# Kernel optimization log

Measured on AMD Instinct MI355X. Metric: run time of the kernel, lower is better.

The kernel has to match this reference:

```python
import jax, jax.numpy as jnp
import numpy as np

N = 100000   # nodes
E = 1600000  # edges
H = 256      # hidden_dim
G = 64       # graphs in batch
OUT = 2      # out_dim


def setup_inputs() -> dict:
    key = jax.random.key(0)
    ks = jax.random.split(key, 20)
    f32 = jnp.float32

    def w(k, shape, fan_in):
        lim = 1.0 / np.sqrt(fan_in)
        return jax.random.uniform(k, shape, f32, -lim, lim)

    return {
        "content_x": jax.random.normal(ks[0], (N, 310), f32),
        "bert_x":    jax.random.normal(ks[1], (N, 768), f32),
        "profile_x": jax.random.normal(ks[2], (N, 10), f32),
        "spacy_x":   jax.random.normal(ks[3], (N, 300), f32),
        "edge_index": jax.random.randint(ks[4], (2, E), 0, N, dtype=jnp.int32),
        "batch":      jax.random.randint(ks[5], (N,), 0, G, dtype=jnp.int32),
        # feature-branch linears
        "Wc": w(ks[6], (310, H), 310), "bc": jnp.zeros((H,), f32),
        "Wb": w(ks[7], (768, H), 768), "bb": jnp.zeros((H,), f32),
        "Wp": w(ks[8], (10, H), 10),   "bp": jnp.zeros((H,), f32),
        "Ws": w(ks[9], (300, H), 300), "bs": jnp.zeros((H,), f32),
        # GCN conv weights (PyG GCNConv: x @ W, aggregate, + bias)
        "Wg1": w(ks[10], (4 * H, H), 4 * H), "bg1": jnp.zeros((H,), f32),
        "Wg2": w(ks[11], (H, H), H),         "bg2": jnp.zeros((H,), f32),
        # head linears
        "Wl1": w(ks[12], (H, H), H),   "bl1": jnp.zeros((H,), f32),
        "Wl2": w(ks[13], (H, OUT), H), "bl2": jnp.zeros((OUT,), f32),
    }


def gcn_conv(x, W, b, src, dst, n_nodes):
    """PyG GCNConv with added self-loops and symmetric normalization."""
    h = x @ W  # [N, out]
    # degree (dst side) including self-loop
    deg = jnp.ones((n_nodes,), h.dtype).at[dst].add(1.0)
    dinv = jax.lax.rsqrt(deg)
    coef = (dinv[src] * dinv[dst])[:, None]          # [E,1]
    agg = jax.ops.segment_sum(h[src] * coef, dst, num_segments=n_nodes)
    agg = agg + h * (dinv * dinv)[:, None]           # self-loop term
    return agg + b


def reference(content_x, bert_x, profile_x, spacy_x, edge_index, batch,
              Wc, bc, Wb, bb, Wp, bp, Ws, bs,
              Wg1, bg1, Wg2, bg2, Wl1, bl1, Wl2, bl2):
    relu = jax.nn.relu
    # multi-branch linear + relu, then concat
    out = jnp.concatenate([
        relu(content_x @ Wc + bc),
        relu(bert_x @ Wb + bb),
        relu(profile_x @ Wp + bp),
        relu(spacy_x @ Ws + bs),
    ], axis=1)  # [N, 4H]
    # dropout is identity at inference
    src, dst = edge_index[0], edge_index[1]
    out = relu(gcn_conv(out, Wg1, bg1, src, dst, N))
    out = relu(gcn_conv(out, Wg2, bg2, src, dst, N))
    # global mean pool over graphs
    ones = jnp.ones((N,), out.dtype)
    cnt = jax.ops.segment_sum(ones, batch, num_segments=G)
    pooled = jax.ops.segment_sum(out, batch, num_segments=G)
    pooled = pooled / jnp.maximum(cnt, 1.0)[:, None]  # [G, H]
    h = relu(pooled @ Wl1 + bl1)
    logits = h @ Wl2 + bl2
    return jax.nn.log_softmax(logits, axis=-1)
```

## Files before the change

kernel.cpp:

```cpp
#include <hip/hip_runtime.h>
#include <hip/hip_bf16.h>
#include <stdint.h>

#define NN 100000
#define NE 1600000
#define HID 256
#define NGRAPH 64
#define POOL_BLOCKS 256

typedef __attribute__((ext_vector_type(8))) short short8;
typedef __attribute__((ext_vector_type(4))) float f32x4;
typedef __attribute__((ext_vector_type(4))) unsigned int u32x4;

static __device__ inline float bf2f(unsigned short u){
  union { unsigned int i; float f; } x; x.i = ((unsigned int)u) << 16; return x.f;
}
static __device__ inline unsigned short f2bf(float f){
  union { float f; unsigned int i; } x; x.f = f;
  unsigned int r = x.i + 0x7fffu + ((x.i >> 16) & 1u);
  return (unsigned short)(r >> 16);
}
static __device__ inline void gload16(const void* g, void* l){
  __builtin_amdgcn_global_load_lds((const __attribute__((address_space(1))) void*)g,
                                   (__attribute__((address_space(3))) void*)l, 16, 0, 0);
}
static __device__ __forceinline__ void fence_bar_v8(){
  asm volatile("s_waitcnt vmcnt(8) lgkmcnt(0)" ::: "memory");
  __builtin_amdgcn_s_barrier(); __builtin_amdgcn_sched_barrier(0);
}
static __device__ __forceinline__ void fence_bar_v4(){
  asm volatile("s_waitcnt vmcnt(4) lgkmcnt(0)" ::: "memory");
  __builtin_amdgcn_s_barrier(); __builtin_amdgcn_sched_barrier(0);
}
static __device__ __forceinline__ void fence_bar_v0(){
  asm volatile("s_waitcnt vmcnt(0) lgkmcnt(0)" ::: "memory");
  __builtin_amdgcn_s_barrier(); __builtin_amdgcn_sched_barrier(0);
}

struct GArgs {
  const void* A;
  const unsigned short* WT;
  const float* bias;
  unsigned short* C;
  int lda, K, Kp, ldc;
};

__global__ __launch_bounds__(256) void gemmf_k(GArgs g0, GArgs g1, GArgs g2, GArgs g3, int M)
{
  __shared__ unsigned char smem[2][16384];
  GArgs g = g0;
  if (blockIdx.z == 1) g = g1;
  else if (blockIdx.z == 2) g = g2;
  else if (blockIdx.z == 3) g = g3;

  const int tid = threadIdx.x, lane = tid & 63, wid = tid >> 6;
  const int wm = wid >> 1, wn = wid & 1;
  const int bm = blockIdx.x * 128, bn = blockIdx.y * 128;
  const int l15 = lane & 15, lk = lane >> 4;
  const int K = g.K, Kp = g.Kp, lda = g.lda, NK = Kp >> 5;
  const float* Af = (const float*)g.A;

  size_t rbF[2]; int kcF[2], wbF[2];
#pragma unroll
  for (int it = 0; it < 2; ++it) {
    int cidx = it * 256 + tid, row = cidx >> 2, c = cidx & 3;
    int gr = bm + row; if (gr >= M) gr = M - 1;
    rbF[it] = (size_t)gr * lda; kcF[it] = c * 8;
    wbF[it] = row * 64 + ((c ^ ((row >> 1) & 3)) << 4);
  }
  size_t obB[2]; int ldsB[2];
#pragma unroll
  for (int it = 0; it < 2; ++it) {
    int inst = it * 4 + wid, cidx = inst * 64 + lane, row = cidx >> 2, c = cidx & 3;
    obB[it] = (size_t)(bn + row) * Kp + (c ^ ((row >> 1) & 3)) * 8;
    ldsB[it] = 8192 + inst * 1024;
  }

  float2 fvA[8], fvB[8];
  f32x4 acc[4][4];
#pragma unroll
  for (int i = 0; i < 4; i++)
#pragma unroll
    for (int j = 0; j < 4; j++) acc[i][j] = (f32x4){0.f, 0.f, 0.f, 0.f};

#define LOADF(S, k0_) do{ \
  if ((k0_) + 32 <= K) { \
    _Pragma("unroll") for (int it = 0; it < 2; ++it){ \
      const float* bp = Af + rbF[it] + (k0_) + kcF[it]; \
      _Pragma("unroll") for (int q = 0; q < 4; ++q) S[it*4+q] = *(const float2*)(bp + 2*q); \
    } \
  } else { \
    _Pragma("unroll") for (int it = 0; it < 2; ++it){ \
      const float* bp = Af + rbF[it]; \
      _Pragma("unroll") for (int q = 0; q < 4; ++q){ \
        int k = (k0_) + kcF[it] + 2*q; \
        S[it*4+q].x = (k < K) ? bp[k] : 0.f; \
        S[it*4+q].y = (k+1 < K) ? bp[k+1] : 0.f; \
      } } } } while(0)

#define CVTW(S, bufb) do{ \
  _Pragma("unroll") for (int it = 0; it < 2; ++it){ \
    u32x4 pk; \
    _Pragma("unroll") for (int q = 0; q < 4; ++q) \
      pk[q] = (unsigned)f2bf(S[it*4+q].x) | ((unsigned)f2bf(S[it*4+q].y) << 16); \
    *(u32x4*)(&smem[bufb][wbF[it]]) = pk; } } while(0)

#define STAGEB(bufb, k0_) do{ \
  _Pragma("unroll") for (int it = 0; it < 2; ++it) \
    gload16(g.WT + obB[it] + (k0_), &smem[bufb][ldsB[it]]); } while(0)

#define DOMFMA(bufb) do{ \
  short8 a[4], b[4]; \
  _Pragma("unroll") for (int i = 0; i < 4; ++i){ int row = wm*64 + i*16 + l15; \
    a[i] = *(const short8*)(&smem[bufb][row*64 + ((lk ^ ((row>>1)&3)) << 4)]); } \
  _Pragma("unroll") for (int j = 0; j < 4; ++j){ int row = wn*64 + j*16 + l15; \
    b[j] = *(const short8*)(&smem[bufb][8192 + row*64 + ((lk ^ ((row>>1)&3)) << 4)]); } \
  _Pragma("unroll") for (int i = 0; i < 4; ++i) \
    _Pragma("unroll") for (int j = 0; j < 4; ++j) \
      acc[i][j] = __builtin_amdgcn_mfma_f32_16x16x32_bf16(a[i], b[j], acc[i][j], 0, 0, 0); \
  } while(0)

  LOADF(fvA, 0);
  CVTW(fvA, 0);
  STAGEB(0, 0);
  LOADF(fvB, 32);
  fence_bar_v8();

  for (int t = 0; t < NK; t += 2) {
    { const bool h1 = (t + 1) < NK, h2 = (t + 2) < NK;
      if (h1) STAGEB(1, (t + 1) << 5);
      if (h2) LOADF(fvA, (t + 2) << 5);
      DOMFMA(0);
      if (h1) CVTW(fvB, 1);
      if (h2) fence_bar_v8(); else fence_bar_v0(); }
    { const bool h1 = (t + 2) < NK, h2 = (t + 3) < NK;
      if (h1) STAGEB(0, (t + 2) << 5);
      if (h2) LOADF(fvB, (t + 3) << 5);
      DOMFMA(1);
      if (h1) CVTW(fvA, 0);
      if (h2) fence_bar_v8(); else fence_bar_v0(); }
  }

#pragma unroll
  for (int j = 0; j < 4; j++) {
    int col = bn + wn * 64 + j * 16 + l15;
    float bv = g.bias[col];
#pragma unroll
    for (int i = 0; i < 4; i++) {
#pragma unroll
      for (int r = 0; r < 4; r++) {
        int row = bm + wm * 64 + i * 16 + lk * 4 + r;
        float v = fmaxf(acc[i][j][r] + bv, 0.f);
        unsigned u = f2bf(v);
        unsigned pu = (unsigned)__shfl_xor((int)u, 1);
        if (!(lane & 1) && row < M)
          *(unsigned*)(g.C + (size_t)row * g.ldc + col) = u | (pu << 16);
      }
    }
  }
#undef LOADF
#undef CVTW
#undef STAGEB
#undef DOMFMA
}

__global__ __launch_bounds__(256) void gemmb_k(GArgs g, int M)
{
  __shared__ unsigned char smem[49152];
  const int tid = threadIdx.x, lane = tid & 63, wid = tid >> 6;
  const int wm = wid >> 1, wn = wid & 1;
  const int bm = blockIdx.x * 128, bn = blockIdx.y * 128;
  const int l15 = lane & 15, lk = lane >> 4;
  const int Kp = g.Kp, lda = g.lda, NK = Kp >> 5;
  const unsigned short* Ab = (const unsigned short*)g.A;

  size_t obA[2], obB[2]; int ldsA[2], ldsB[2];
#pragma unroll
  for (int it = 0; it < 2; ++it) {
    int inst = it * 4 + wid, cidx = inst * 64 + lane, row = cidx >> 2, c = cidx & 3;
    int gr = bm + row; if (gr >= M) gr = M - 1;
    obA[it] = (size_t)gr * lda + (c ^ ((row >> 1) & 3)) * 8;
    ldsA[it] = inst * 1024;
    obB[it] = (size_t)(bn + row) * Kp + (c ^ ((row >> 1) & 3)) * 8;
    ldsB[it] = 8192 + inst * 1024;
  }

  f32x4 acc[4][4];
#pragma unroll
  for (int i = 0; i < 4; i++)
#pragma unroll
    for (int j = 0; j < 4; j++) acc[i][j] = (f32x4){0.f, 0.f, 0.f, 0.f};

#define STAGE3(ob_, k0_) do{ \
  _Pragma("unroll") for (int it = 0; it < 2; ++it) \
    gload16(Ab + obA[it] + (k0_), smem + (ob_) + ldsA[it]); \
  _Pragma("unroll") for (int it = 0; it < 2; ++it) \
    gload16(g.WT + obB[it] + (k0_), smem + (ob_) + ldsB[it]); } while(0)

  STAGE3(0, 0);
  STAGE3(16384, 32);
  fence_bar_v4();
  int o0 = 0, o1 = 16384, o2 = 32768;

  for (int t = 0; t < NK; ++t) {
    const bool h2 = (t + 2) < NK;
    if (h2) STAGE3(o2, (t + 2) << 5);
    short8 a[4], b[4];
#pragma unroll
    for (int i = 0; i < 4; ++i) { int row = wm * 64 + i * 16 + l15;
      a[i] = *(const short8*)(smem + o0 + row * 64 + ((lk ^ ((row >> 1) & 3)) << 4)); }
#pragma unroll
    for (int j = 0; j < 4; ++j) { int row = wn * 64 + j * 16 + l15;
      b[j] = *(const short8*)(smem + o0 + 8192 + row * 64 + ((lk ^ ((row >> 1) & 3)) << 4)); }
#pragma unroll
    for (int i = 0; i < 4; ++i)
#pragma unroll
      for (int j = 0; j < 4; ++j)
        acc[i][j] = __builtin_amdgcn_mfma_f32_16x16x32_bf16(a[i], b[j], acc[i][j], 0, 0, 0);
    if (h2) fence_bar_v4(); else fence_bar_v0();
    int tmp = o0; o0 = o1; o1 = o2; o2 = tmp;
  }

#pragma unroll
  for (int j = 0; j < 4; j++) {
    int col = bn + wn * 64 + j * 16 + l15;
#pragma unroll
    for (int i = 0; i < 4; i++) {
#pragma unroll
      for (int r = 0; r < 4; r++) {
        int row = bm + wm * 64 + i * 16 + lk * 4 + r;
        unsigned u = f2bf(acc[i][j][r]);
        unsigned pu = (unsigned)__shfl_xor((int)u, 1);
        if (!(lane & 1) && row < M)
          *(unsigned*)(g.C + (size_t)row * g.ldc + col) = u | (pu << 16);
      }
    }
  }
#undef STAGE3
}

__global__ void wconv_k(const float* __restrict__ W, unsigned short* __restrict__ WT,
                        int K, int Kp)
{
  int idx = blockIdx.x * 256 + threadIdx.x;
  if (idx >= 256 * Kp) return;
  int n = idx / Kp, k = idx - n * Kp;
  float v = (k < K) ? W[(size_t)k * 256 + n] : 0.f;
  WT[(size_t)n * Kp + k] = f2bf(v);
}

__global__ void zero_int_k(int* p, int n){
  int i = blockIdx.x * 256 + threadIdx.x; if (i < n) p[i] = 0;
}
__global__ void count_k(const int* __restrict__ dst, int* __restrict__ cnt, int n){
  int e = blockIdx.x * 256 + threadIdx.x; if (e < n) atomicAdd(&cnt[dst[e]], 1);
}
__global__ void deg_k(const int* __restrict__ cnt, float* __restrict__ dinv,
                      float* __restrict__ selfc, int n){
  int i = blockIdx.x * 256 + threadIdx.x;
  if (i < n) { float d = 1.0f + (float)cnt[i]; dinv[i] = rsqrtf(d); selfc[i] = 1.0f / d; }
}
__global__ void scan1_k(const int* __restrict__ cnt, int* __restrict__ bsum, int n){
  __shared__ int s[256];
  int b = blockIdx.x, t = threadIdx.x;
  int base = b * 1024 + t * 4, v = 0;
#pragma unroll
  for (int j = 0; j < 4; j++) { int i = base + j; if (i < n) v += cnt[i]; }
  s[t] = v; __syncthreads();
  for (int o = 128; o > 0; o >>= 1) { if (t < o) s[t] += s[t + o]; __syncthreads(); }
  if (t == 0) bsum[b] = s[0];
}
__global__ void scan2_k(int* bsum, int nb){
  __shared__ int s[256];
  int t = threadIdx.x;
  int v = (t < nb) ? bsum[t] : 0;
  s[t] = v; __syncthreads();
  for (int o = 1; o < 256; o <<= 1) {
    int x = (t >= o) ? s[t - o] : 0; __syncthreads();
    s[t] += x; __syncthreads();
  }
  if (t < nb) bsum[t] = s[t] - v;
}
__global__ void scan3_k(const int* __restrict__ cnt, const int* __restrict__ bsum,
                        int* __restrict__ rowstart, int* __restrict__ cursor, int n){
  __shared__ int s[256];
  int b = blockIdx.x, t = threadIdx.x;
  int base = b * 1024 + t * 4;
  int c0 = 0, c1 = 0, c2 = 0, c3 = 0;
  if (base + 0 < n) c0 = cnt[base + 0];
  if (base + 1 < n) c1 = cnt[base + 1];
  if (base + 2 < n) c2 = cnt[base + 2];
  if (base + 3 < n) c3 = cnt[base + 3];
  int ts = c0 + c1 + c2 + c3;
  s[t] = ts; __syncthreads();
  for (int o = 1; o < 256; o <<= 1) {
    int x = (t >= o) ? s[t - o] : 0; __syncthreads();
    s[t] += x; __syncthreads();
  }
  int run = bsum[b] + s[t] - ts;
  int cc[4] = {c0, c1, c2, c3};
#pragma unroll
  for (int j = 0; j < 4; j++) {
    int i = base + j;
    if (i < n) {
      rowstart[i] = run; cursor[i] = run; run += cc[j];
      if (i == n - 1) rowstart[n] = run;
    }
  }
}
__global__ void scatter_k(const int* __restrict__ src, const int* __restrict__ dst,
                          const float* __restrict__ dinv, int* __restrict__ cursor,
                          int* __restrict__ csr_src, float* __restrict__ csr_coef, int n){
  int e = blockIdx.x * 256 + threadIdx.x; if (e >= n) return;
  int d = dst[e], s = src[e];
  int p = atomicAdd(&cursor[d], 1);
  csr_src[p] = s;
  csr_coef[p] = dinv[s] * dinv[d];
}

__global__ __launch_bounds__(256) void agg_k(
    const unsigned short* __restrict__ h,
    const int* __restrict__ rowstart, const int* __restrict__ csr_src,
    const float* __restrict__ csr_coef, const float* __restrict__ selfc,
    const float* __restrict__ bias, unsigned short* __restrict__ out)
{
  int dst = blockIdx.x * 4 + (threadIdx.x >> 6);
  if (dst >= NN) return;
  int lane = threadIdx.x & 63;
  int colb = lane * 4;
  const unsigned short* hb = h + colb;
  ushort4 hv = *(const ushort4*)(hb + (size_t)dst * 256);
  float sc = selfc[dst];
  float a0 = sc * bf2f(hv.x), a1 = sc * bf2f(hv.y), a2 = sc * bf2f(hv.z), a3 = sc * bf2f(hv.w);
  int e0 = rowstart[dst], e1 = rowstart[dst + 1];
  int e = e0;
  for (; e + 8 <= e1; e += 8) {
    int ss[8]; float cc[8]; ushort4 vv[8];
#pragma unroll
    for (int q = 0; q < 8; ++q) { ss[q] = csr_src[e + q]; cc[q] = csr_coef[e + q]; }
#pragma unroll
    for (int q = 0; q < 8; ++q) vv[q] = *(const ushort4*)(hb + (size_t)ss[q] * 256);
#pragma unroll
    for (int q = 0; q < 8; ++q) {
      a0 += cc[q] * bf2f(vv[q].x); a1 += cc[q] * bf2f(vv[q].y);
      a2 += cc[q] * bf2f(vv[q].z); a3 += cc[q] * bf2f(vv[q].w);
    }
  }
  for (; e + 2 <= e1; e += 2) {
    int s0 = csr_src[e], s1 = csr_src[e + 1];
    float c0 = csr_coef[e], c1 = csr_coef[e + 1];
    ushort4 v0 = *(const ushort4*)(hb + (size_t)s0 * 256);
    ushort4 v1 = *(const ushort4*)(hb + (size_t)s1 * 256);
    a0 += c0 * bf2f(v0.x) + c1 * bf2f(v1.x); a1 += c0 * bf2f(v0.y) + c1 * bf2f(v1.y);
    a2 += c0 * bf2f(v0.z) + c1 * bf2f(v1.z); a3 += c0 * bf2f(v0.w) + c1 * bf2f(v1.w);
  }
  if (e < e1) {
    int s0 = csr_src[e]; float c0 = csr_coef[e];
    ushort4 v0 = *(const ushort4*)(hb + (size_t)s0 * 256);
    a0 += c0 * bf2f(v0.x); a1 += c0 * bf2f(v0.y); a2 += c0 * bf2f(v0.z); a3 += c0 * bf2f(v0.w);
  }
  float4 bv = *(const float4*)(bias + colb);
  a0 = fmaxf(a0 + bv.x, 0.f); a1 = fmaxf(a1 + bv.y, 0.f);
  a2 = fmaxf(a2 + bv.z, 0.f); a3 = fmaxf(a3 + bv.w, 0.f);
  ushort4 o; o.x = f2bf(a0); o.y = f2bf(a1); o.z = f2bf(a2); o.w = f2bf(a3);
  *(ushort4*)(out + (size_t)dst * 256 + colb) = o;
}

__global__ __launch_bounds__(256) void pool_k(
    const unsigned short* __restrict__ x, const int* __restrict__ batch,
    float* __restrict__ pp, float* __restrict__ cp)
{
  __shared__ float acc[NGRAPH][HID];
  __shared__ float cl[NGRAPH];
  int t = threadIdx.x, b = blockIdx.x;
  for (int i = t; i < NGRAPH * HID; i += 256) ((float*)acc)[i] = 0.f;
  if (t < NGRAPH) cl[t] = 0.f;
  __syncthreads();
  int per = (NN + POOL_BLOCKS - 1) / POOL_BLOCKS;
  int i0 = b * per, i1 = min(NN, i0 + per);
  for (int i = i0; i < i1; ++i) {
    int g = batch[i];
    acc[g][t] += bf2f(x[(size_t)i * 256 + t]);
    if (t == 0) cl[g] += 1.f;
  }
  __syncthreads();
  for (int g = 0; g < NGRAPH; ++g) pp[(size_t)b * (NGRAPH * HID) + g * HID + t] = acc[g][t];
  if (t < NGRAPH) cp[b * NGRAPH + t] = cl[t];
}

__global__ __launch_bounds__(256) void head_k(
    const float* __restrict__ pp, const float* __restrict__ cp,
    const float* __restrict__ Wl1, const float* __restrict__ bl1,
    const float* __restrict__ Wl2, const float* __restrict__ bl2,
    float* __restrict__ out)
{
  __shared__ float pooled[HID];
  __shared__ float red[2][4];
  int g = blockIdx.x, t = threadIdx.x;
  float s = 0.f;
  for (int b = 0; b < POOL_BLOCKS; ++b) s += pp[(size_t)b * (NGRAPH * HID) + g * HID + t];
  float cnt = 0.f;
  for (int b = 0; b < POOL_BLOCKS; ++b) cnt += cp[b * NGRAPH + g];
  pooled[t] = s / fmaxf(cnt, 1.f);
  __syncthreads();
  float hv = bl1[t];
  for (int k = 0; k < HID; ++k) hv += pooled[k] * Wl1[k * HID + t];
  hv = fmaxf(hv, 0.f);
  float p0 = hv * Wl2[t * 2 + 0];
  float p1 = hv * Wl2[t * 2 + 1];
  for (int o = 32; o > 0; o >>= 1) { p0 += __shfl_down(p0, o); p1 += __shfl_down(p1, o); }
  int w = t >> 6;
  if ((t & 63) == 0) { red[0][w] = p0; red[1][w] = p1; }
  __syncthreads();
  if (t == 0) {
    float l0 = bl2[0], l1 = bl2[1];
#pragma unroll
    for (int i = 0; i < 4; i++) { l0 += red[0][i]; l1 += red[1][i]; }
    float m = fmaxf(l0, l1);
    float lse = m + logf(expf(l0 - m) + expf(l1 - m));
    out[g * 2 + 0] = l0 - lse;
    out[g * 2 + 1] = l1 - lse;
  }
}

extern "C" void kernel_launch(void* const* d_in, const int* in_sizes, int n_in,
                              void* d_out, int out_size, void* d_ws, size_t ws_size,
                              hipStream_t stream)
{
  const float* content = (const float*)d_in[0];
  const float* bert    = (const float*)d_in[1];
  const float* profile = (const float*)d_in[2];
  const float* spacy   = (const float*)d_in[3];
  const int*   eidx    = (const int*)d_in[4];
  const int*   batch   = (const int*)d_in[5];
  const float* Wc = (const float*)d_in[6];  const float* bc = (const float*)d_in[7];
  const float* Wb = (const float*)d_in[8];  const float* bb = (const float*)d_in[9];
  const float* Wp = (const float*)d_in[10]; const float* bp = (const float*)d_in[11];
  const float* Ws = (const float*)d_in[12]; const float* bs = (const float*)d_in[13];
  const float* Wg1 = (const float*)d_in[14]; const float* bg1 = (const float*)d_in[15];
  const float* Wg2 = (const float*)d_in[16]; const float* bg2 = (const float*)d_in[17];
  const float* Wl1 = (const float*)d_in[18]; const float* bl1 = (const float*)d_in[19];
  const float* Wl2 = (const float*)d_in[20]; const float* bl2 = (const float*)d_in[21];
  float* out = (float*)d_out;
  const int* srcp = eidx;
  const int* dstp = eidx + NE;

  const int KPC = 320, KPB = 768, KPP = 64, KPS = 320, KPG1 = 1024, KPG2 = 256;

  char* ws = (char*)d_ws;
  size_t off = 0;
  auto alloc = [&](size_t bytes) { size_t o = off; off += (bytes + 255) & ~(size_t)255; return o; };

  unsigned short* WTc  = (unsigned short*)(ws + alloc((size_t)256 * KPC * 2));
  unsigned short* WTb  = (unsigned short*)(ws + alloc((size_t)256 * KPB * 2));
  unsigned short* WTp  = (unsigned short*)(ws + alloc((size_t)256 * KPP * 2));
  unsigned short* WTs  = (unsigned short*)(ws + alloc((size_t)256 * KPS * 2));
  unsigned short* WTg1 = (unsigned short*)(ws + alloc((size_t)256 * KPG1 * 2));
  unsigned short* WTg2 = (unsigned short*)(ws + alloc((size_t)256 * KPG2 * 2));
  float* dinv    = (float*)(ws + alloc((size_t)NN * 4));
  float* selfc   = (float*)(ws + alloc((size_t)NN * 4));
  int* rowcnt    = (int*)(ws + alloc((size_t)NN * 4));
  int* rowstart  = (int*)(ws + alloc((size_t)(NN + 1) * 4));
  int* cursor    = (int*)(ws + alloc((size_t)NN * 4));
  int* csr_src   = (int*)(ws + alloc((size_t)NE * 4));
  float* csr_coef= (float*)(ws + alloc((size_t)NE * 4));
  int* bsum      = (int*)(ws + alloc(1024));
  float* pp      = (float*)(ws + alloc((size_t)POOL_BLOCKS * NGRAPH * HID * 4));
  float* cp      = (float*)(ws + alloc((size_t)POOL_BLOCKS * NGRAPH * 4));
  unsigned short* X1 = (unsigned short*)(ws + alloc((size_t)NN * 1024 * 2));
  unsigned short* H  = (unsigned short*)(ws + alloc((size_t)NN * 256 * 2));
  unsigned short* X2 = (unsigned short*)(ws + alloc((size_t)NN * 256 * 2));
  unsigned short* X3 = (unsigned short*)(ws + alloc((size_t)NN * 256 * 2));
  (void)ws_size; (void)in_sizes; (void)n_in; (void)out_size;

  hipStream_t s = stream;
  const int NB = (NN + 1023) / 1024;
  const int MB = (NN + 127) / 128;

  wconv_k<<<(256 * KPC + 255) / 256, 256, 0, s>>>(Wc, WTc, 310, KPC);
  wconv_k<<<(256 * KPB + 255) / 256, 256, 0, s>>>(Wb, WTb, 768, KPB);
  wconv_k<<<(256 * KPP + 255) / 256, 256, 0, s>>>(Wp, WTp, 10, KPP);
  wconv_k<<<(256 * KPS + 255) / 256, 256, 0, s>>>(Ws, WTs, 300, KPS);
  wconv_k<<<(256 * KPG1 + 255) / 256, 256, 0, s>>>(Wg1, WTg1, 1024, KPG1);
  wconv_k<<<(256 * KPG2 + 255) / 256, 256, 0, s>>>(Wg2, WTg2, 256, KPG2);

  zero_int_k<<<(NN + 255) / 256, 256, 0, s>>>(rowcnt, NN);
  count_k<<<(NE + 255) / 256, 256, 0, s>>>(dstp, rowcnt, NE);
  deg_k<<<(NN + 255) / 256, 256, 0, s>>>(rowcnt, dinv, selfc, NN);
  scan1_k<<<NB, 256, 0, s>>>(rowcnt, bsum, NN);
  scan2_k<<<1, 256, 0, s>>>(bsum, NB);
  scan3_k<<<NB, 256, 0, s>>>(rowcnt, bsum, rowstart, cursor, NN);
  scatter_k<<<(NE + 255) / 256, 256, 0, s>>>(srcp, dstp, dinv, cursor, csr_src, csr_coef, NE);

  {
    GArgs gc = { content, WTc, bc, X1 + 0,   310, 310, KPC, 1024 };
    GArgs gb = { bert,    WTb, bb, X1 + 256, 768, 768, KPB, 1024 };
    GArgs gp = { profile, WTp, bp, X1 + 512, 10,  10,  KPP, 1024 };
    GArgs gs = { spacy,   WTs, bs, X1 + 768, 300, 300, KPS, 1024 };
    gemmf_k<<<dim3(MB, 2, 4), 256, 0, s>>>(gc, gb, gp, gs, NN);
  }

  {
    GArgs g1 = { X1, WTg1, nullptr, H, 1024, 1024, KPG1, 256 };
    gemmb_k<<<dim3(MB, 2, 1), 256, 0, s>>>(g1, NN);
  }
  agg_k<<<(NN + 3) / 4, 256, 0, s>>>(H, rowstart, csr_src, csr_coef, selfc, bg1, X2);

  {
    GArgs g2 = { X2, WTg2, nullptr, H, 256, 256, KPG2, 256 };
    gemmb_k<<<dim3(MB, 2, 1), 256, 0, s>>>(g2, NN);
  }
  agg_k<<<(NN + 3) / 4, 256, 0, s>>>(H, rowstart, csr_src, csr_coef, selfc, bg2, X3);

  pool_k<<<POOL_BLOCKS, 256, 0, s>>>(X3, batch, pp, cp);
  head_k<<<NGRAPH, 256, 0, s>>>(pp, cp, Wl1, bl1, Wl2, bl2, out);
}
```

Baseline: 1.544 ms.

## Load GEMM operands directly to registers instead of staging through LDS

Both GEMM kernels drop shared-memory staging and barriers. Each lane now loads its MFMA A and B fragments straight from global memory into a register double buffer, and in the fp32-input GEMM converts with the packed v_cvt_pk_bf16_f32 instruction. The grid swaps x and y so both N-tiles of a row block run next to each other for L2 reuse of A, and launch bounds raise occupancy hints. The feature GEMM is split into two launches (aligned and unaligned inputs), with vectorized 16-byte loads on the aligned pair. Risks are uncoalesced strided global loads with duplicated traffic across waves, plus register pressure.

```diff
diff --git a/kernel.cpp b/kernel.cpp
--- a/kernel.cpp
+++ b/kernel.cpp
@@ -10,7 +10,7 @@
 
 typedef __attribute__((ext_vector_type(8))) short short8;
 typedef __attribute__((ext_vector_type(4))) float f32x4;
-typedef __attribute__((ext_vector_type(4))) unsigned int u32x4;
+typedef __attribute__((ext_vector_type(2))) float f32x2;
 
 static __device__ inline float bf2f(unsigned short u){
   union { unsigned int i; float f; } x; x.i = ((unsigned int)u) << 16; return x.f;
@@ -19,22 +19,6 @@
   union { float f; unsigned int i; } x; x.f = f;
   unsigned int r = x.i + 0x7fffu + ((x.i >> 16) & 1u);
   return (unsigned short)(r >> 16);
-}
-static __device__ inline void gload16(const void* g, void* l){
-  __builtin_amdgcn_global_load_lds((const __attribute__((address_space(1))) void*)g,
-                                   (__attribute__((address_space(3))) void*)l, 16, 0, 0);
-}
-static __device__ __forceinline__ void fence_bar_v8(){
-  asm volatile("s_waitcnt vmcnt(8) lgkmcnt(0)" ::: "memory");
-  __builtin_amdgcn_s_barrier(); __builtin_amdgcn_sched_barrier(0);
-}
-static __device__ __forceinline__ void fence_bar_v4(){
-  asm volatile("s_waitcnt vmcnt(4) lgkmcnt(0)" ::: "memory");
-  __builtin_amdgcn_s_barrier(); __builtin_amdgcn_sched_barrier(0);
-}
-static __device__ __forceinline__ void fence_bar_v0(){
-  asm volatile("s_waitcnt vmcnt(0) lgkmcnt(0)" ::: "memory");
-  __builtin_amdgcn_s_barrier(); __builtin_amdgcn_sched_barrier(0);
 }
 
 struct GArgs {
@@ -45,100 +29,84 @@
   int lda, K, Kp, ldc;
 };
 
-__global__ __launch_bounds__(256) void gemmf_k(GArgs g0, GArgs g1, GArgs g2, GArgs g3, int M)
-{
-  __shared__ unsigned char smem[2][16384];
-  GArgs g = g0;
-  if (blockIdx.z == 1) g = g1;
-  else if (blockIdx.z == 2) g = g2;
-  else if (blockIdx.z == 3) g = g3;
-
+template<bool AL4>
+__global__ __launch_bounds__(256, 2) void gemmf_k(GArgs g0, GArgs g1, int M)
+{
+  GArgs g = (blockIdx.z == 0) ? g0 : g1;
   const int tid = threadIdx.x, lane = tid & 63, wid = tid >> 6;
   const int wm = wid >> 1, wn = wid & 1;
-  const int bm = blockIdx.x * 128, bn = blockIdx.y * 128;
+  const int bm = blockIdx.y * 128, bn = blockIdx.x * 128;
   const int l15 = lane & 15, lk = lane >> 4;
   const int K = g.K, Kp = g.Kp, lda = g.lda, NK = Kp >> 5;
-  const float* Af = (const float*)g.A;
-
-  size_t rbF[2]; int kcF[2], wbF[2];
-#pragma unroll
-  for (int it = 0; it < 2; ++it) {
-    int cidx = it * 256 + tid, row = cidx >> 2, c = cidx & 3;
-    int gr = bm + row; if (gr >= M) gr = M - 1;
-    rbF[it] = (size_t)gr * lda; kcF[it] = c * 8;
-    wbF[it] = row * 64 + ((c ^ ((row >> 1) & 3)) << 4);
-  }
-  size_t obB[2]; int ldsB[2];
-#pragma unroll
-  for (int it = 0; it < 2; ++it) {
-    int inst = it * 4 + wid, cidx = inst * 64 + lane, row = cidx >> 2, c = cidx & 3;
-    obB[it] = (size_t)(bn + row) * Kp + (c ^ ((row >> 1) & 3)) * 8;
-    ldsB[it] = 8192 + inst * 1024;
-  }
-
-  float2 fvA[8], fvB[8];
+  const float* __restrict__ Af = (const float*)g.A;
+  const unsigned short* __restrict__ WT = g.WT;
+  const int kb = lk * 8;
+
+  unsigned rbF[4];
+#pragma unroll
+  for (int i = 0; i < 4; ++i) {
+    int gr = bm + wm * 64 + i * 16 + l15; if (gr >= M) gr = M - 1;
+    rbF[i] = (unsigned)gr * (unsigned)lda;
+  }
+  unsigned obB[4];
+#pragma unroll
+  for (int j = 0; j < 4; ++j)
+    obB[j] = (unsigned)(bn + wn * 64 + j * 16 + l15) * (unsigned)Kp;
+
+  f32x2 a0[16], a1[16];
+  short8 b0[4], b1[4];
   f32x4 acc[4][4];
 #pragma unroll
   for (int i = 0; i < 4; i++)
 #pragma unroll
     for (int j = 0; j < 4; j++) acc[i][j] = (f32x4){0.f, 0.f, 0.f, 0.f};
 
-#define LOADF(S, k0_) do{ \
+#define LOADA(S, k0_) do{ \
   if ((k0_) + 32 <= K) { \
-    _Pragma("unroll") for (int it = 0; it < 2; ++it){ \
-      const float* bp = Af + rbF[it] + (k0_) + kcF[it]; \
-      _Pragma("unroll") for (int q = 0; q < 4; ++q) S[it*4+q] = *(const float2*)(bp + 2*q); \
+    if (AL4) { \
+      _Pragma("unroll") for (int i = 0; i < 4; ++i){ \
+        const float* p = Af + rbF[i] + (k0_) + kb; \
+        f32x4 v0 = *(const f32x4*)p, v1 = *(const f32x4*)(p + 4); \
+        S[i*4+0] = (f32x2){v0.x, v0.y}; S[i*4+1] = (f32x2){v0.z, v0.w}; \
+        S[i*4+2] = (f32x2){v1.x, v1.y}; S[i*4+3] = (f32x2){v1.z, v1.w}; } \
+    } else { \
+      _Pragma("unroll") for (int i = 0; i < 4; ++i){ \
+        const float* p = Af + rbF[i] + (k0_) + kb; \
+        _Pragma("unroll") for (int q = 0; q < 4; ++q) S[i*4+q] = *(const f32x2*)(p + 2*q); } \
     } \
   } else { \
-    _Pragma("unroll") for (int it = 0; it < 2; ++it){ \
-      const float* bp = Af + rbF[it]; \
+    _Pragma("unroll") for (int i = 0; i < 4; ++i){ \
+      const float* p = Af + rbF[i]; \
       _Pragma("unroll") for (int q = 0; q < 4; ++q){ \
-        int k = (k0_) + kcF[it] + 2*q; \
-        S[it*4+q].x = (k < K) ? bp[k] : 0.f; \
-        S[it*4+q].y = (k+1 < K) ? bp[k+1] : 0.f; \
-      } } } } while(0)
-
-#define CVTW(S, bufb) do{ \
-  _Pragma("unroll") for (int it = 0; it < 2; ++it){ \
-    u32x4 pk; \
+        int k = (k0_) + kb + 2*q; \
+        S[i*4+q].x = (k < K) ? p[k] : 0.f; \
+        S[i*4+q].y = (k + 1 < K) ? p[k+1] : 0.f; } } \
+  } } while(0)
+
+#define LOADB(S, k0_) do{ \
+  _Pragma("unroll") for (int j = 0; j < 4; ++j) \
+    S[j] = *(const short8*)(WT + obB[j] + (k0_) + kb); } while(0)
+
+#define CVTMFMA(S, B) do{ \
+  short8 af[4]; \
+  _Pragma("unroll") for (int i = 0; i < 4; ++i){ \
+    union { short8 s; unsigned u[4]; } t; \
     _Pragma("unroll") for (int q = 0; q < 4; ++q) \
-      pk[q] = (unsigned)f2bf(S[it*4+q].x) | ((unsigned)f2bf(S[it*4+q].y) << 16); \
-    *(u32x4*)(&smem[bufb][wbF[it]]) = pk; } } while(0)
-
-#define STAGEB(bufb, k0_) do{ \
-  _Pragma("unroll") for (int it = 0; it < 2; ++it) \
-    gload16(g.WT + obB[it] + (k0_), &smem[bufb][ldsB[it]]); } while(0)
-
-#define DOMFMA(bufb) do{ \
-  short8 a[4], b[4]; \
-  _Pragma("unroll") for (int i = 0; i < 4; ++i){ int row = wm*64 + i*16 + l15; \
-    a[i] = *(const short8*)(&smem[bufb][row*64 + ((lk ^ ((row>>1)&3)) << 4)]); } \
-  _Pragma("unroll") for (int j = 0; j < 4; ++j){ int row = wn*64 + j*16 + l15; \
-    b[j] = *(const short8*)(&smem[bufb][8192 + row*64 + ((lk ^ ((row>>1)&3)) << 4)]); } \
+      asm("v_cvt_pk_bf16_f32 %0, %1, %2" : "=v"(t.u[q]) : "v"(S[i*4+q].x), "v"(S[i*4+q].y)); \
+    af[i] = t.s; } \
   _Pragma("unroll") for (int i = 0; i < 4; ++i) \
     _Pragma("unroll") for (int j = 0; j < 4; ++j) \
-      acc[i][j] = __builtin_amdgcn_mfma_f32_16x16x32_bf16(a[i], b[j], acc[i][j], 0, 0, 0); \
+      acc[i][j] = __builtin_amdgcn_mfma_f32_16x16x32_bf16(af[i], B[j], acc[i][j], 0, 0, 0); \
   } while(0)
 
-  LOADF(fvA, 0);
-  CVTW(fvA, 0);
-  STAGEB(0, 0);
-  LOADF(fvB, 32);
-  fence_bar_v8();
+  LOADA(a0, 0); LOADB(b0, 0);
+  if (NK > 1) { LOADA(a1, 32); LOADB(b1, 32); }
 
   for (int t = 0; t < NK; t += 2) {
-    { const bool h1 = (t + 1) < NK, h2 = (t + 2) < NK;
-      if (h1) STAGEB(1, (t + 1) << 5);
-      if (h2) LOADF(fvA, (t + 2) << 5);
-      DOMFMA(0);
-      if (h1) CVTW(fvB, 1);
-      if (h2) fence_bar_v8(); else fence_bar_v0(); }
-    { const bool h1 = (t + 2) < NK, h2 = (t + 3) < NK;
-      if (h1) STAGEB(0, (t + 2) << 5);
-      if (h2) LOADF(fvB, (t + 3) << 5);
-      DOMFMA(1);
-      if (h1) CVTW(fvA, 0);
-      if (h2) fence_bar_v8(); else fence_bar_v0(); }
+    { CVTMFMA(a0, b0);
+      if (t + 2 < NK) { LOADA(a0, (t + 2) << 5); LOADB(b0, (t + 2) << 5); } }
+    { CVTMFMA(a1, b1);
+      if (t + 3 < NK) { LOADA(a1, (t + 3) << 5); LOADB(b1, (t + 3) << 5); } }
   }
 
 #pragma unroll
@@ -158,67 +126,58 @@
       }
     }
   }
-#undef LOADF
-#undef CVTW
-#undef STAGEB
-#undef DOMFMA
-}
-
-__global__ __launch_bounds__(256) void gemmb_k(GArgs g, int M)
-{
-  __shared__ unsigned char smem[49152];
+#undef LOADA
+#undef LOADB
+#undef CVTMFMA
+}
+
+__global__ __launch_bounds__(256, 3) void gemmb_k(GArgs g, int M)
+{
   const int tid = threadIdx.x, lane = tid & 63, wid = tid >> 6;
   const int wm = wid >> 1, wn = wid & 1;
-  const int bm = blockIdx.x * 128, bn = blockIdx.y * 128;
+  const int bm = blockIdx.y * 128, bn = blockIdx.x * 128;
   const int l15 = lane & 15, lk = lane >> 4;
   const int Kp = g.Kp, lda = g.lda, NK = Kp >> 5;
-  const unsigned short* Ab = (const unsigned short*)g.A;
-
-  size_t obA[2], obB[2]; int ldsA[2], ldsB[2];
-#pragma unroll
-  for (int it = 0; it < 2; ++it) {
-    int inst = it * 4 + wid, cidx = inst * 64 + lane, row = cidx >> 2, c = cidx & 3;
-    int gr = bm + row; if (gr >= M) gr = M - 1;
-    obA[it] = (size_t)gr * lda + (c ^ ((row >> 1) & 3)) * 8;
-    ldsA[it] = inst * 1024;
-    obB[it] = (size_t)(bn + row) * Kp + (c ^ ((row >> 1) & 3)) * 8;
-    ldsB[it] = 8192 + inst * 1024;
-  }
-
+  const unsigned short* __restrict__ Ab = (const unsigned short*)g.A;
+  const unsigned short* __restrict__ WT = g.WT;
+  const int kb = lk * 8;
+
+  unsigned rbA[4];
+#pragma unroll
+  for (int i = 0; i < 4; ++i) {
+    int gr = bm + wm * 64 + i * 16 + l15; if (gr >= M) gr = M - 1;
+    rbA[i] = (unsigned)gr * (unsigned)lda;
+  }
+  unsigned obB[4];
+#pragma unroll
+  for (int j = 0; j < 4; ++j)
+    obB[j] = (unsigned)(bn + wn * 64 + j * 16 + l15) * (unsigned)Kp;
+
+  short8 a0[4], a1[4], b0[4], b1[4];
   f32x4 acc[4][4];
 #pragma unroll
   for (int i = 0; i < 4; i++)
 #pragma unroll
     for (int j = 0; j < 4; j++) acc[i][j] = (f32x4){0.f, 0.f, 0.f, 0.f};
 
-#define STAGE3(ob_, k0_) do{ \
-  _Pragma("unroll") for (int it = 0; it < 2; ++it) \
-    gload16(Ab + obA[it] + (k0_), smem + (ob_) + ldsA[it]); \
-  _Pragma("unroll") for (int it = 0; it < 2; ++it) \
-    gload16(g.WT + obB[it] + (k0_), smem + (ob_) + ldsB[it]); } while(0)
-
-  STAGE3(0, 0);
-  STAGE3(16384, 32);
-  fence_bar_v4();
-  int o0 = 0, o1 = 16384, o2 = 32768;
-
-  for (int t = 0; t < NK; ++t) {
-    const bool h2 = (t + 2) < NK;
-    if (h2) STAGE3(o2, (t + 2) << 5);
-    short8 a[4], b[4];
-#pragma unroll
-    for (int i = 0; i < 4; ++i) { int row = wm * 64 + i * 16 + l15;
-      a[i] = *(const short8*)(smem + o0 + row * 64 + ((lk ^ ((row >> 1) & 3)) << 4)); }
-#pragma unroll
-    for (int j = 0; j < 4; ++j) { int row = wn * 64 + j * 16 + l15;
-      b[j] = *(const short8*)(smem + o0 + 8192 + row * 64 + ((lk ^ ((row >> 1) & 3)) << 4)); }
-#pragma unroll
-    for (int i = 0; i < 4; ++i)
-#pragma unroll
-      for (int j = 0; j < 4; ++j)
-        acc[i][j] = __builtin_amdgcn_mfma_f32_16x16x32_bf16(a[i], b[j], acc[i][j], 0, 0, 0);
-    if (h2) fence_bar_v4(); else fence_bar_v0();
-    int tmp = o0; o0 = o1; o1 = o2; o2 = tmp;
+#define LOADAB(SA, SB, k0_) do{ \
+  _Pragma("unroll") for (int i = 0; i < 4; ++i) \
+    SA[i] = *(const short8*)(Ab + rbA[i] + (k0_) + kb); \
+  _Pragma("unroll") for (int j = 0; j < 4; ++j) \
+    SB[j] = *(const short8*)(WT + obB[j] + (k0_) + kb); } while(0)
+
+#define DOMFMA(SA, SB) do{ \
+  _Pragma("unroll") for (int i = 0; i < 4; ++i) \
+    _Pragma("unroll") for (int j = 0; j < 4; ++j) \
+      acc[i][j] = __builtin_amdgcn_mfma_f32_16x16x32_bf16(SA[i], SB[j], acc[i][j], 0, 0, 0); \
+  } while(0)
+
+  LOADAB(a0, b0, 0);
+  if (NK > 1) LOADAB(a1, b1, 32);
+
+  for (int t = 0; t < NK; t += 2) {
+    { DOMFMA(a0, b0); if (t + 2 < NK) LOADAB(a0, b0, (t + 2) << 5); }
+    { DOMFMA(a1, b1); if (t + 3 < NK) LOADAB(a1, b1, (t + 3) << 5); }
   }
 
 #pragma unroll
@@ -236,7 +195,8 @@
       }
     }
   }
-#undef STAGE3
+#undef LOADAB
+#undef DOMFMA
 }
 
 __global__ void wconv_k(const float* __restrict__ W, unsigned short* __restrict__ WT,
@@ -493,22 +453,23 @@
   scatter_k<<<(NE + 255) / 256, 256, 0, s>>>(srcp, dstp, dinv, cursor, csr_src, csr_coef, NE);
 
   {
+    GArgs gb = { bert,    WTb, bb, X1 + 256, 768, 768, KPB, 1024 };
+    GArgs gs = { spacy,   WTs, bs, X1 + 768, 300, 300, KPS, 1024 };
     GArgs gc = { content, WTc, bc, X1 + 0,   310, 310, KPC, 1024 };
-    GArgs gb = { bert,    WTb, bb, X1 + 256, 768, 768, KPB, 1024 };
     GArgs gp = { profile, WTp, bp, X1 + 512, 10,  10,  KPP, 1024 };
-    GArgs gs = { spacy,   WTs, bs, X1 + 768, 300, 300, KPS, 1024 };
-    gemmf_k<<<dim3(MB, 2, 4), 256, 0, s>>>(gc, gb, gp, gs, NN);
+    gemmf_k<true ><<<dim3(2, MB, 2), 256, 0, s>>>(gb, gs, NN);
+    gemmf_k<false><<<dim3(2, MB, 2), 256, 0, s>>>(gc, gp, NN);
   }
 
   {
     GArgs g1 = { X1, WTg1, nullptr, H, 1024, 1024, KPG1, 256 };
-    gemmb_k<<<dim3(MB, 2, 1), 256, 0, s>>>(g1, NN);
+    gemmb_k<<<dim3(2, MB), 256, 0, s>>>(g1, NN);
   }
   agg_k<<<(NN + 3) / 4, 256, 0, s>>>(H, rowstart, csr_src, csr_coef, selfc, bg1, X2);
 
   {
     GArgs g2 = { X2, WTg2, nullptr, H, 256, 256, KPG2, 256 };
-    gemmb_k<<<dim3(MB, 2, 1), 256, 0, s>>>(g2, NN);
+    gemmb_k<<<dim3(2, MB), 256, 0, s>>>(g2, NN);
   }
   agg_k<<<(NN + 3) / 4, 256, 0, s>>>(H, rowstart, csr_src, csr_coef, selfc, bg2, X3);
 
```

Result: slower. 1.828 ms (+18.4%).
